# Kernel tuning notes

Hardware: AMD Instinct MI355X
Metric: run time of the kernel (lower is better)

## Reference

```python
import jax, jax.numpy as jnp
import numpy as np

HIDDEN_DIM = 2048
NUM_HEADS = 16
HEAD_DIM = HIDDEN_DIM // NUM_HEADS


def setup_inputs() -> dict:
    key = jax.random.key(0)
    ks = jax.random.split(key, 5)
    B, S, D = 1, 4096, HIDDEN_DIM
    scale = 1.0 / np.sqrt(D)
    x = jax.random.normal(ks[0], (B, S, D), dtype=jnp.float32)
    w_q = jax.random.normal(ks[1], (D, D), dtype=jnp.float32) * scale
    w_k = jax.random.normal(ks[2], (D, D), dtype=jnp.float32) * scale
    w_v = jax.random.normal(ks[3], (D, D), dtype=jnp.float32) * scale
    w_o = jax.random.normal(ks[4], (D, D), dtype=jnp.float32) * scale
    return {"x": x, "w_q": w_q, "w_k": w_k, "w_v": w_v, "w_o": w_o, "causal": 1}


def reference(x, w_q, w_k, w_v, w_o, causal):
    B, S, D = x.shape
    H, Dh = NUM_HEADS, HEAD_DIM
    sm_scale = 1.0 / np.sqrt(Dh)

    # projections (x @ W.T)
    q = jnp.einsum('bsd,ed->bse', x, w_q).reshape(B, S, H, Dh).transpose(0, 2, 1, 3)
    k = jnp.einsum('bsd,ed->bse', x, w_k).reshape(B, S, H, Dh).transpose(0, 2, 1, 3)
    v = jnp.einsum('bsd,ed->bse', x, w_v).reshape(B, S, H, Dh).transpose(0, 2, 1, 3)

    # attention scores [B, H, S, S]; flash online-softmax == standard softmax
    scores = jnp.einsum('bhqd,bhkd->bhqk', q, k) * sm_scale
    if causal:
        qpos = jnp.arange(S)[:, None]
        kpos = jnp.arange(S)[None, :]
        scores = jnp.where(qpos >= kpos, scores, -jnp.inf)
    probs = jax.nn.softmax(scores, axis=-1)
    o = jnp.einsum('bhqk,bhkd->bhqd', probs, v)  # [B, H, S, Dh]
    o = o.transpose(0, 2, 1, 3).reshape(B, S, D)
    return jnp.einsum('bsd,ed->bse', o, w_o)
```

## Files before the change

kernel.cpp:

```cpp
#include <hip/hip_runtime.h>
#include <stdint.h>

typedef __bf16 bf16_t;
typedef __bf16 bf16x8 __attribute__((ext_vector_type(8)));
typedef __bf16 bf16x4 __attribute__((ext_vector_type(4)));
typedef float  f32x4  __attribute__((ext_vector_type(4)));

static constexpr int S  = 4096;
static constexpr int D  = 2048;
static constexpr int H  = 16;
static constexpr int DH = 128;

__device__ __forceinline__ bf16x8 ld8(const bf16_t* p) { return *(const bf16x8*)p; }
__device__ __forceinline__ bf16x8 ld8c(const float* p) {
  const f32x4 a = *(const f32x4*)p;
  const f32x4 b = *(const f32x4*)(p + 4);
  bf16x8 r;
  r[0] = (bf16_t)a[0]; r[1] = (bf16_t)a[1]; r[2] = (bf16_t)a[2]; r[3] = (bf16_t)a[3];
  r[4] = (bf16_t)b[0]; r[5] = (bf16_t)b[1]; r[6] = (bf16_t)b[2]; r[7] = (bf16_t)b[3];
  return r;
}

__device__ __forceinline__ void async_ld16(const bf16_t* g, bf16_t* lds) {
  __builtin_amdgcn_global_load_lds(
      (const __attribute__((address_space(1))) uint32_t*)g,
      (__attribute__((address_space(3))) uint32_t*)lds, 16, 0, 0);
}

__global__ __launch_bounds__(256) void cvt_kernel(
    const float* __restrict__ x,  const float* __restrict__ wq,
    const float* __restrict__ wk, const float* __restrict__ wv,
    const float* __restrict__ wo,
    bf16_t* __restrict__ xb,  bf16_t* __restrict__ wqb,
    bf16_t* __restrict__ wkb, bf16_t* __restrict__ wvb,
    bf16_t* __restrict__ wob) {
  const int z = blockIdx.z;
  const float* src; bf16_t* dst; size_t off = 0;
  if      (z == 0) { src = x;  dst = xb;  off = 0; }
  else if (z == 1) { src = x;  dst = xb;  off = 4194304; }
  else if (z == 2) { src = wq; dst = wqb; }
  else if (z == 3) { src = wk; dst = wkb; }
  else if (z == 4) { src = wv; dst = wvb; }
  else             { src = wo; dst = wob; }
  const size_t i = off + ((size_t)blockIdx.x * 256 + threadIdx.x) * 8;
  *(bf16x8*)(dst + i) = ld8c(src + i);
}

template <typename TC, bool TR>
__device__ __forceinline__ void gemm_async(const bf16_t* __restrict__ A,
                                           const bf16_t* __restrict__ W,
                                           TC* __restrict__ C) {
  constexpr int K  = D;
  constexpr int BK = 32;
  __shared__ __align__(16) bf16_t Ash[128 * BK];
  __shared__ __align__(16) bf16_t Bsh[128 * BK];
  const int tid = threadIdx.x;
  const int w = tid >> 6, lane = tid & 63;
  const int c = lane & 15, g = lane >> 4;
  const int wm = w >> 1, wn = w & 1;
  const int rowBase = blockIdx.y * 128;
  const int colBase = blockIdx.x * 128;

  f32x4 acc[4][4] = {};

  for (int k0 = 0; k0 < K; k0 += BK) {
    __syncthreads();
    #pragma unroll
    for (int r = 0; r < 2; ++r) {
      const int cid = r * 256 + tid;
      const int row = cid >> 2, q = cid & 3;
      async_ld16(A + (size_t)(rowBase + row) * K + k0 + q * 8,
                 Ash + r * 2048 + w * 512);
      async_ld16(W + (size_t)(colBase + row) * K + k0 + q * 8,
                 Bsh + r * 2048 + w * 512);
    }
    __syncthreads();

    bf16x8 af[4], bf[4];
    #pragma unroll
    for (int i = 0; i < 4; ++i) af[i] = ld8(Ash + (wm * 64 + i * 16 + c) * BK + g * 8);
    #pragma unroll
    for (int j = 0; j < 4; ++j) bf[j] = ld8(Bsh + (wn * 64 + j * 16 + c) * BK + g * 8);
    #pragma unroll
    for (int i = 0; i < 4; ++i)
      #pragma unroll
      for (int j = 0; j < 4; ++j)
        acc[i][j] = __builtin_amdgcn_mfma_f32_16x16x32_bf16(af[i], bf[j], acc[i][j], 0, 0, 0);
  }

  #pragma unroll
  for (int i = 0; i < 4; ++i)
    #pragma unroll
    for (int j = 0; j < 4; ++j) {
      if (TR) {
        const int col  = colBase + wn * 64 + j * 16 + c;
        const int row0 = rowBase + wm * 64 + i * 16 + g * 4;
        bf16x4 v;
        #pragma unroll
        for (int r = 0; r < 4; ++r) v[r] = (bf16_t)acc[i][j][r];
        *(bf16x4*)((bf16_t*)C + (size_t)col * S + row0) = v;
      } else {
        #pragma unroll
        for (int r = 0; r < 4; ++r) {
          const int row = rowBase + wm * 64 + i * 16 + g * 4 + r;
          const int col = colBase + wn * 64 + j * 16 + c;
          C[(size_t)row * D + col] = (TC)acc[i][j][r];
        }
      }
    }
}

__global__ __launch_bounds__(256) void qkv_gemm_bf16(
    const bf16_t* __restrict__ X,
    const bf16_t* __restrict__ Wq, const bf16_t* __restrict__ Wk,
    const bf16_t* __restrict__ Wv,
    bf16_t* __restrict__ Qo, bf16_t* __restrict__ Ko, bf16_t* __restrict__ VTo,
    int* __restrict__ ctr) {
  if (blockIdx.x == 0 && blockIdx.y == 0 && blockIdx.z == 0 && threadIdx.x == 0)
    atomicExch(ctr, 0);
  if (blockIdx.z == 0)      gemm_async<bf16_t, false>(X, Wq, Qo);
  else if (blockIdx.z == 1) gemm_async<bf16_t, false>(X, Wk, Ko);
  else                      gemm_async<bf16_t, true >(X, Wv, VTo);
}

__global__ __launch_bounds__(256) void out_gemm_bf16(
    const bf16_t* __restrict__ A, const bf16_t* __restrict__ W,
    float* __restrict__ C) {
  gemm_async<float, false>(A, W, C);
}

__global__ __launch_bounds__(256, 2) void attn_kernel(
    const bf16_t* __restrict__ Q, const bf16_t* __restrict__ Kb,
    const bf16_t* __restrict__ VTg, bf16_t* __restrict__ O,
    const int* __restrict__ causal_p, int* __restrict__ ctr) {
  constexpr int LDK = 40;
  __shared__ __align__(16) bf16_t Ksh[4 * 64 * LDK];
  __shared__ __align__(16) bf16_t Vt[2 * 128 * LDK];
  __shared__ __align__(16) bf16_t Psh[4 * 2 * 32 * LDK];
  __shared__ int item_s;

  const int tid = threadIdx.x, w = tid >> 6, lane = tid & 63;
  const int c = lane & 15, g = lane >> 4;
  const int causal = causal_p[0];
  constexpr float QS = 0.08838834764831845f * 1.4426950408889634f;

  int knA[4], d0A[4], dV[4], kcV[4];
  #pragma unroll
  for (int r = 0; r < 4; ++r) {
    const int cid = r * 256 + tid;
    knA[r] = cid >> 4; d0A[r] = (cid & 15) * 8;
    dV[r]  = cid >> 3; kcV[r] = cid & 7;
  }

  bf16x8 onesf;
  #pragma unroll
  for (int e = 0; e < 8; ++e) onesf[e] = (c == 0) ? (bf16_t)1.0f : (bf16_t)0.0f;

  while (true) {
    __syncthreads();
    if (tid == 0) item_s = atomicAdd(ctr, 1);
    __syncthreads();
    const int it = item_s;
    if (it >= 512) break;
    const int t = causal ? (31 - (it >> 4)) : (it >> 4);
    const int h = it & 15;
    const int wrow = t * 128 + w * 32;
    const int ktiles = causal ? (2 * t + 2) : 64;

    bf16x8 qf[2][4];
    #pragma unroll
    for (int i = 0; i < 2; ++i)
      #pragma unroll
      for (int kf = 0; kf < 4; ++kf) {
        const bf16x8 raw = ld8(Q + (size_t)(wrow + i * 16 + c) * D + h * DH + kf * 32 + g * 8);
        bf16x8 sc;
        #pragma unroll
        for (int e = 0; e < 8; ++e) sc[e] = (bf16_t)((float)raw[e] * QS);
        qf[i][kf] = sc;
      }

    f32x4 o_acc[2][8] = {};
    f32x4 o_l[2] = {};

    bf16x8 kreg[4], vreg[4];
    #pragma unroll
    for (int r = 0; r < 4; ++r) {
      kreg[r] = ld8(Kb + (size_t)(0 + knA[r]) * D + h * DH + d0A[r]);
      vreg[r] = ld8(VTg + (size_t)(h * DH + dV[r]) * S + 0 + kcV[r] * 8);
    }

    for (int kt = 0; kt < ktiles; ++kt) {
      __syncthreads();
      #pragma unroll
      for (int r = 0; r < 4; ++r) {
        *(bf16x8*)(Ksh + (d0A[r] >> 5) * (64 * LDK) + knA[r] * LDK + (d0A[r] & 31)) = kreg[r];
        *(bf16x8*)(Vt + (kcV[r] >> 2) * (128 * LDK) + dV[r] * LDK + (kcV[r] & 3) * 8) = vreg[r];
      }
      __syncthreads();
      if (kt + 1 < ktiles) {
        #pragma unroll
        for (int r = 0; r < 4; ++r) {
          kreg[r] = ld8(Kb + (size_t)((kt + 1) * 64 + knA[r]) * D + h * DH + d0A[r]);
          vreg[r] = ld8(VTg + (size_t)(h * DH + dV[r]) * S + (kt + 1) * 64 + kcV[r] * 8);
        }
      }

      const bool active = !causal || (kt * 64 <= wrow + 31);
      if (active) {
        f32x4 s[2][4] = {};
        #pragma unroll
        for (int nf = 0; nf < 4; ++nf) {
          bf16x8 kk[4];
          #pragma unroll
          for (int kf = 0; kf < 4; ++kf)
            kk[kf] = ld8(Ksh + kf * (64 * LDK) + (nf * 16 + c) * LDK + g * 8);
          #pragma unroll
          for (int i = 0; i < 2; ++i)
            #pragma unroll
            for (int kf = 0; kf < 4; ++kf)
              s[i][nf] = __builtin_amdgcn_mfma_f32_16x16x32_bf16(qf[i][kf], kk[kf], s[i][nf], 0, 0, 0);
        }

        if (causal && (kt * 64 + 63 > wrow)) {
          #pragma unroll
          for (int i = 0; i < 2; ++i)
            #pragma unroll
            for (int nf = 0; nf < 4; ++nf)
              #pragma unroll
              for (int r = 0; r < 4; ++r) {
                const int kc2 = kt * 64 + nf * 16 + c;
                const int qr = wrow + i * 16 + g * 4 + r;
                if (kc2 > qr) s[i][nf][r] = -1e30f;
              }
        }

        #pragma unroll
        for (int i = 0; i < 2; ++i)
          #pragma unroll
          for (int r = 0; r < 4; ++r) {
            const int qr = i * 16 + g * 4 + r;
            #pragma unroll
            for (int nf = 0; nf < 4; ++nf) {
              const float pv = exp2f(s[i][nf][r]);
              Psh[w * (2 * 32 * LDK) + (nf >> 1) * (32 * LDK) + qr * LDK + (nf & 1) * 16 + c] = (bf16_t)pv;
            }
          }

        #pragma unroll
        for (int kf2 = 0; kf2 < 2; ++kf2) {
          bf16x8 pf[2];
          #pragma unroll
          for (int i = 0; i < 2; ++i)
            pf[i] = ld8(Psh + w * (2 * 32 * LDK) + kf2 * (32 * LDK) + (i * 16 + c) * LDK + g * 8);
          #pragma unroll
          for (int i = 0; i < 2; ++i)
            o_l[i] = __builtin_amdgcn_mfma_f32_16x16x32_bf16(pf[i], onesf, o_l[i], 0, 0, 0);
          #pragma unroll
          for (int nf = 0; nf < 8; ++nf) {
            const bf16x8 vf = ld8(Vt + kf2 * (128 * LDK) + (nf * 16 + c) * LDK + g * 8);
            #pragma unroll
            for (int i = 0; i < 2; ++i)
              o_acc[i][nf] = __builtin_amdgcn_mfma_f32_16x16x32_bf16(pf[i], vf, o_acc[i][nf], 0, 0, 0);
          }
        }
      }
    }

    #pragma unroll
    for (int i = 0; i < 2; ++i)
      #pragma unroll
      for (int r = 0; r < 4; ++r) {
        const float lv = __shfl(o_l[i][r], lane & 48, 64);
        const float inv = 1.0f / lv;
        const int row = wrow + i * 16 + g * 4 + r;
        #pragma unroll
        for (int nf = 0; nf < 8; ++nf)
          O[(size_t)row * D + h * DH + nf * 16 + c] = (bf16_t)(o_acc[i][nf][r] * inv);
      }
  }
}

extern "C" void kernel_launch(void* const* d_in, const int* in_sizes, int n_in,
                              void* d_out, int out_size, void* d_ws, size_t ws_size,
                              hipStream_t stream) {
  const float* x  = (const float*)d_in[0];
  const float* wq = (const float*)d_in[1];
  const float* wk = (const float*)d_in[2];
  const float* wv = (const float*)d_in[3];
  const float* wo = (const float*)d_in[4];
  const int* causal = (const int*)d_in[5];
  float* out = (float*)d_out;

  bf16_t* Qb  = (bf16_t*)d_ws;
  bf16_t* Kb  = Qb + (size_t)S * D;
  bf16_t* VTb = Kb + (size_t)S * D;
  bf16_t* Ob  = VTb + (size_t)S * D;
  bf16_t* xb  = Ob + (size_t)S * D;
  bf16_t* wqb = xb + (size_t)S * D;
  bf16_t* wkb = wqb + (size_t)D * D;
  bf16_t* wvb = wkb + (size_t)D * D;
  bf16_t* wob = wvb + (size_t)D * D;
  int*    ctr = (int*)(wob + (size_t)D * D);

  dim3 blk(256);
  cvt_kernel<<<dim3(2048, 1, 6), blk, 0, stream>>>(x, wq, wk, wv, wo,
                                                   xb, wqb, wkb, wvb, wob);
  qkv_gemm_bf16<<<dim3(D / 128, S / 128, 3), blk, 0, stream>>>(xb, wqb, wkb, wvb,
                                                               Qb, Kb, VTb, ctr);
  attn_kernel<<<dim3(512), blk, 0, stream>>>(Qb, Kb, VTb, Ob, causal, ctr);
  out_gemm_bf16<<<dim3(D / 128, S / 128), blk, 0, stream>>>(Ob, wob, out);
}
```

Measured before the change: 448.6 us.

## Split attention key tile across wave pairs with LDS reduction of partial outputs

The attention block grows to 512 threads (8 waves). Each pair of waves shares a 32-row query slice and takes one 32-column half of each 64-key tile, and the two partial O and row-sum accumulators are combined through LDS in two phases at the end. The causal work order also changes from longest-first to a mixed schedule. The goal is more waves in flight to hide latency and finer causal skipping per half tile. In exchange it adds extra syncs and an LDS reduction, and the new launch bounds may constrain registers.

```diff
diff --git a/kernel.cpp b/kernel.cpp
--- a/kernel.cpp
+++ b/kernel.cpp
@@ -129,25 +129,27 @@
   gemm_async<float, false>(A, W, C);
 }
 
-__global__ __launch_bounds__(256, 2) void attn_kernel(
+__global__ __launch_bounds__(512, 4) void attn_kernel(
     const bf16_t* __restrict__ Q, const bf16_t* __restrict__ Kb,
     const bf16_t* __restrict__ VTg, bf16_t* __restrict__ O,
     const int* __restrict__ causal_p, int* __restrict__ ctr) {
   constexpr int LDK = 40;
-  __shared__ __align__(16) bf16_t Ksh[4 * 64 * LDK];
-  __shared__ __align__(16) bf16_t Vt[2 * 128 * LDK];
-  __shared__ __align__(16) bf16_t Psh[4 * 2 * 32 * LDK];
+  __shared__ __align__(16) bf16_t smem[(4 * 64 + 2 * 128 + 8 * 32) * LDK];
+  bf16_t* const Ksh = smem;
+  bf16_t* const Vt  = smem + 4 * 64 * LDK;
+  bf16_t* const Psh = smem + (4 * 64 + 2 * 128) * LDK;
   __shared__ int item_s;
 
   const int tid = threadIdx.x, w = tid >> 6, lane = tid & 63;
   const int c = lane & 15, g = lane >> 4;
+  const int wq = w >> 1, wk = w & 1;
   const int causal = causal_p[0];
   constexpr float QS = 0.08838834764831845f * 1.4426950408889634f;
 
-  int knA[4], d0A[4], dV[4], kcV[4];
+  int knA[2], d0A[2], dV[2], kcV[2];
   #pragma unroll
-  for (int r = 0; r < 4; ++r) {
-    const int cid = r * 256 + tid;
+  for (int r = 0; r < 2; ++r) {
+    const int cid = r * 512 + tid;
     knA[r] = cid >> 4; d0A[r] = (cid & 15) * 8;
     dV[r]  = cid >> 3; kcV[r] = cid & 7;
   }
@@ -155,6 +157,8 @@
   bf16x8 onesf;
   #pragma unroll
   for (int e = 0; e < 8; ++e) onesf[e] = (c == 0) ? (bf16_t)1.0f : (bf16_t)0.0f;
+
+  bf16_t* const PshW = Psh + w * (32 * LDK);
 
   while (true) {
     __syncthreads();
@@ -162,9 +166,10 @@
     __syncthreads();
     const int it = item_s;
     if (it >= 512) break;
-    const int t = causal ? (31 - (it >> 4)) : (it >> 4);
+    const int jj = it >> 4;
+    const int t = causal ? ((jj < 16) ? (31 - jj) : (jj - 16)) : jj;
     const int h = it & 15;
-    const int wrow = t * 128 + w * 32;
+    const int wrow = t * 128 + wq * 32;
     const int ktiles = causal ? (2 * t + 2) : 64;
 
     bf16x8 qf[2][4];
@@ -182,53 +187,49 @@
     f32x4 o_acc[2][8] = {};
     f32x4 o_l[2] = {};
 
-    bf16x8 kreg[4], vreg[4];
-    #pragma unroll
-    for (int r = 0; r < 4; ++r) {
-      kreg[r] = ld8(Kb + (size_t)(0 + knA[r]) * D + h * DH + d0A[r]);
-      vreg[r] = ld8(VTg + (size_t)(h * DH + dV[r]) * S + 0 + kcV[r] * 8);
+    bf16x8 kreg[2], vreg[2];
+    #pragma unroll
+    for (int r = 0; r < 2; ++r) {
+      kreg[r] = ld8(Kb + (size_t)knA[r] * D + h * DH + d0A[r]);
+      vreg[r] = ld8(VTg + (size_t)(h * DH + dV[r]) * S + kcV[r] * 8);
     }
 
     for (int kt = 0; kt < ktiles; ++kt) {
       __syncthreads();
       #pragma unroll
-      for (int r = 0; r < 4; ++r) {
+      for (int r = 0; r < 2; ++r) {
         *(bf16x8*)(Ksh + (d0A[r] >> 5) * (64 * LDK) + knA[r] * LDK + (d0A[r] & 31)) = kreg[r];
         *(bf16x8*)(Vt + (kcV[r] >> 2) * (128 * LDK) + dV[r] * LDK + (kcV[r] & 3) * 8) = vreg[r];
       }
       __syncthreads();
       if (kt + 1 < ktiles) {
         #pragma unroll
-        for (int r = 0; r < 4; ++r) {
+        for (int r = 0; r < 2; ++r) {
           kreg[r] = ld8(Kb + (size_t)((kt + 1) * 64 + knA[r]) * D + h * DH + d0A[r]);
           vreg[r] = ld8(VTg + (size_t)(h * DH + dV[r]) * S + (kt + 1) * 64 + kcV[r] * 8);
         }
       }
 
-      const bool active = !causal || (kt * 64 <= wrow + 31);
+      const bool active = !causal || (kt * 64 + wk * 32 <= wrow + 31);
       if (active) {
-        f32x4 s[2][4] = {};
-        #pragma unroll
-        for (int nf = 0; nf < 4; ++nf) {
-          bf16x8 kk[4];
-          #pragma unroll
-          for (int kf = 0; kf < 4; ++kf)
-            kk[kf] = ld8(Ksh + kf * (64 * LDK) + (nf * 16 + c) * LDK + g * 8);
+        f32x4 s[2][2] = {};
+        #pragma unroll
+        for (int nf = 0; nf < 2; ++nf)
+          #pragma unroll
+          for (int kf = 0; kf < 4; ++kf) {
+            const bf16x8 kk = ld8(Ksh + kf * (64 * LDK) + (wk * 32 + nf * 16 + c) * LDK + g * 8);
+            s[0][nf] = __builtin_amdgcn_mfma_f32_16x16x32_bf16(qf[0][kf], kk, s[0][nf], 0, 0, 0);
+            s[1][nf] = __builtin_amdgcn_mfma_f32_16x16x32_bf16(qf[1][kf], kk, s[1][nf], 0, 0, 0);
+          }
+
+        if (causal && (kt * 64 + wk * 32 + 31 > wrow)) {
           #pragma unroll
           for (int i = 0; i < 2; ++i)
             #pragma unroll
-            for (int kf = 0; kf < 4; ++kf)
-              s[i][nf] = __builtin_amdgcn_mfma_f32_16x16x32_bf16(qf[i][kf], kk[kf], s[i][nf], 0, 0, 0);
-        }
-
-        if (causal && (kt * 64 + 63 > wrow)) {
-          #pragma unroll
-          for (int i = 0; i < 2; ++i)
-            #pragma unroll
-            for (int nf = 0; nf < 4; ++nf)
+            for (int nf = 0; nf < 2; ++nf)
               #pragma unroll
               for (int r = 0; r < 4; ++r) {
-                const int kc2 = kt * 64 + nf * 16 + c;
+                const int kc2 = kt * 64 + wk * 32 + nf * 16 + c;
                 const int qr = wrow + i * 16 + g * 4 + r;
                 if (kc2 > qr) s[i][nf][r] = -1e30f;
               }
@@ -240,43 +241,68 @@
           for (int r = 0; r < 4; ++r) {
             const int qr = i * 16 + g * 4 + r;
             #pragma unroll
-            for (int nf = 0; nf < 4; ++nf) {
+            for (int nf = 0; nf < 2; ++nf) {
               const float pv = exp2f(s[i][nf][r]);
-              Psh[w * (2 * 32 * LDK) + (nf >> 1) * (32 * LDK) + qr * LDK + (nf & 1) * 16 + c] = (bf16_t)pv;
+              PshW[qr * LDK + nf * 16 + c] = (bf16_t)pv;
             }
           }
 
-        #pragma unroll
-        for (int kf2 = 0; kf2 < 2; ++kf2) {
-          bf16x8 pf[2];
+        bf16x8 pf[2];
+        #pragma unroll
+        for (int i = 0; i < 2; ++i)
+          pf[i] = ld8(PshW + (i * 16 + c) * LDK + g * 8);
+        #pragma unroll
+        for (int i = 0; i < 2; ++i)
+          o_l[i] = __builtin_amdgcn_mfma_f32_16x16x32_bf16(pf[i], onesf, o_l[i], 0, 0, 0);
+        #pragma unroll
+        for (int nf = 0; nf < 8; ++nf) {
+          const bf16x8 vf = ld8(Vt + wk * (128 * LDK) + (nf * 16 + c) * LDK + g * 8);
           #pragma unroll
           for (int i = 0; i < 2; ++i)
-            pf[i] = ld8(Psh + w * (2 * 32 * LDK) + kf2 * (32 * LDK) + (i * 16 + c) * LDK + g * 8);
-          #pragma unroll
-          for (int i = 0; i < 2; ++i)
-            o_l[i] = __builtin_amdgcn_mfma_f32_16x16x32_bf16(pf[i], onesf, o_l[i], 0, 0, 0);
-          #pragma unroll
-          for (int nf = 0; nf < 8; ++nf) {
-            const bf16x8 vf = ld8(Vt + kf2 * (128 * LDK) + (nf * 16 + c) * LDK + g * 8);
-            #pragma unroll
-            for (int i = 0; i < 2; ++i)
-              o_acc[i][nf] = __builtin_amdgcn_mfma_f32_16x16x32_bf16(pf[i], vf, o_acc[i][nf], 0, 0, 0);
-          }
-        }
-      }
-    }
-
-    #pragma unroll
-    for (int i = 0; i < 2; ++i)
+            o_acc[i][nf] = __builtin_amdgcn_mfma_f32_16x16x32_bf16(pf[i], vf, o_acc[i][nf], 0, 0, 0);
+        }
+      }
+    }
+
+    float* const scratch = (float*)smem;
+    float* const myslot = scratch + (size_t)((wq & 1) * 64 + lane) * 72;
+    #pragma unroll
+    for (int phase = 0; phase < 2; ++phase) {
+      __syncthreads();
+      if ((wq >> 1) == phase && wk == 1) {
+        #pragma unroll
+        for (int i = 0; i < 2; ++i) {
+          #pragma unroll
+          for (int nf = 0; nf < 8; ++nf)
+            *(f32x4*)(myslot + (i * 8 + nf) * 4) = o_acc[i][nf];
+          *(f32x4*)(myslot + 64 + i * 4) = o_l[i];
+        }
+      }
+      __syncthreads();
+      if ((wq >> 1) == phase && wk == 0) {
+        #pragma unroll
+        for (int i = 0; i < 2; ++i) {
+          #pragma unroll
+          for (int nf = 0; nf < 8; ++nf)
+            o_acc[i][nf] += *(const f32x4*)(myslot + (i * 8 + nf) * 4);
+          o_l[i] += *(const f32x4*)(myslot + 64 + i * 4);
+        }
+      }
+    }
+
+    if (wk == 0) {
       #pragma unroll
-      for (int r = 0; r < 4; ++r) {
-        const float lv = __shfl(o_l[i][r], lane & 48, 64);
-        const float inv = 1.0f / lv;
-        const int row = wrow + i * 16 + g * 4 + r;
-        #pragma unroll
-        for (int nf = 0; nf < 8; ++nf)
-          O[(size_t)row * D + h * DH + nf * 16 + c] = (bf16_t)(o_acc[i][nf][r] * inv);
-      }
+      for (int i = 0; i < 2; ++i)
+        #pragma unroll
+        for (int r = 0; r < 4; ++r) {
+          const float lv = __shfl(o_l[i][r], lane & 48, 64);
+          const float inv = 1.0f / lv;
+          const int row = wrow + i * 16 + g * 4 + r;
+          #pragma unroll
+          for (int nf = 0; nf < 8; ++nf)
+            O[(size_t)row * D + h * DH + nf * 16 + c] = (bf16_t)(o_acc[i][nf][r] * inv);
+        }
+    }
   }
 }
 
@@ -307,6 +333,6 @@
                                                    xb, wqb, wkb, wvb, wob);
   qkv_gemm_bf16<<<dim3(D / 128, S / 128, 3), blk, 0, stream>>>(xb, wqb, wkb, wvb,
                                                                Qb, Kb, VTb, ctr);
-  attn_kernel<<<dim3(512), blk, 0, stream>>>(Qb, Kb, VTb, Ob, causal, ctr);
+  attn_kernel<<<dim3(512), dim3(512), 0, stream>>>(Qb, Kb, VTb, Ob, causal, ctr);
   out_gemm_bf16<<<dim3(D / 128, S / 128), blk, 0, stream>>>(Ob, wob, out);
 }
```

Result: slower. 961.8 us (+114.4%).

## Make attention warps independent with per-warp work items and direct global K/V loads

Applied to the files above, without the earlier changes.

Each warp now claims its own 32-row query block through a lane-0 atomic, instead of a 256-thread block claiming a 128-row tile. K and V fragments are read straight from global memory into registers, which removes the shared K/V staging and both __syncthreads per key tile. The goal is to drop block-wide barriers and let each warp stop at its own causal bound, which balances work better. In exchange, K/V reuse across the four warps of a block now relies on L1/L2 instead of LDS, and the global reads are strided and less coalesced.

```diff
diff --git a/kernel.cpp b/kernel.cpp
--- a/kernel.cpp
+++ b/kernel.cpp
@@ -134,38 +134,37 @@
     const bf16_t* __restrict__ VTg, bf16_t* __restrict__ O,
     const int* __restrict__ causal_p, int* __restrict__ ctr) {
   constexpr int LDK = 40;
-  __shared__ __align__(16) bf16_t Ksh[4 * 64 * LDK];
-  __shared__ __align__(16) bf16_t Vt[2 * 128 * LDK];
   __shared__ __align__(16) bf16_t Psh[4 * 2 * 32 * LDK];
-  __shared__ int item_s;
 
   const int tid = threadIdx.x, w = tid >> 6, lane = tid & 63;
   const int c = lane & 15, g = lane >> 4;
   const int causal = causal_p[0];
   constexpr float QS = 0.08838834764831845f * 1.4426950408889634f;
 
-  int knA[4], d0A[4], dV[4], kcV[4];
-  #pragma unroll
-  for (int r = 0; r < 4; ++r) {
-    const int cid = r * 256 + tid;
-    knA[r] = cid >> 4; d0A[r] = (cid & 15) * 8;
-    dV[r]  = cid >> 3; kcV[r] = cid & 7;
-  }
-
   bf16x8 onesf;
   #pragma unroll
   for (int e = 0; e < 8; ++e) onesf[e] = (c == 0) ? (bf16_t)1.0f : (bf16_t)0.0f;
 
+  bf16_t* const PshW = Psh + w * (2 * 32 * LDK);
+
   while (true) {
-    __syncthreads();
-    if (tid == 0) item_s = atomicAdd(ctr, 1);
-    __syncthreads();
-    const int it = item_s;
-    if (it >= 512) break;
-    const int t = causal ? (31 - (it >> 4)) : (it >> 4);
-    const int h = it & 15;
-    const int wrow = t * 128 + w * 32;
-    const int ktiles = causal ? (2 * t + 2) : 64;
+    int it;
+    if (lane == 0) it = atomicAdd(ctr, 1);
+    it = __shfl(it, 0, 64);
+    if (it >= 2048) break;
+
+    int rg, h;
+    if (causal) {
+      const int q = it >> 2, sub = it & 3;
+      const int u = q & 255, hi = q >> 8;
+      const int rq = hi ? (u & 31) : (31 - (u & 31));
+      h  = (hi << 3) | (u >> 5);
+      rg = rq * 4 + sub;
+    } else {
+      h = it >> 7; rg = it & 127;
+    }
+    const int wrow = rg * 32;
+    const int ktiles = causal ? ((wrow >> 6) + 1) : (S / 64);
 
     bf16x8 qf[2][4];
     #pragma unroll
@@ -182,86 +181,64 @@
     f32x4 o_acc[2][8] = {};
     f32x4 o_l[2] = {};
 
-    bf16x8 kreg[4], vreg[4];
-    #pragma unroll
-    for (int r = 0; r < 4; ++r) {
-      kreg[r] = ld8(Kb + (size_t)(0 + knA[r]) * D + h * DH + d0A[r]);
-      vreg[r] = ld8(VTg + (size_t)(h * DH + dV[r]) * S + 0 + kcV[r] * 8);
-    }
-
     for (int kt = 0; kt < ktiles; ++kt) {
-      __syncthreads();
-      #pragma unroll
-      for (int r = 0; r < 4; ++r) {
-        *(bf16x8*)(Ksh + (d0A[r] >> 5) * (64 * LDK) + knA[r] * LDK + (d0A[r] & 31)) = kreg[r];
-        *(bf16x8*)(Vt + (kcV[r] >> 2) * (128 * LDK) + dV[r] * LDK + (kcV[r] & 3) * 8) = vreg[r];
-      }
-      __syncthreads();
-      if (kt + 1 < ktiles) {
+      f32x4 s[2][4] = {};
+      #pragma unroll
+      for (int nf = 0; nf < 4; ++nf) {
+        bf16x8 kk[4];
+        #pragma unroll
+        for (int kf = 0; kf < 4; ++kf)
+          kk[kf] = ld8(Kb + (size_t)(kt * 64 + nf * 16 + c) * D + h * DH + kf * 32 + g * 8);
+        #pragma unroll
+        for (int kf = 0; kf < 4; ++kf) {
+          s[0][nf] = __builtin_amdgcn_mfma_f32_16x16x32_bf16(qf[0][kf], kk[kf], s[0][nf], 0, 0, 0);
+          s[1][nf] = __builtin_amdgcn_mfma_f32_16x16x32_bf16(qf[1][kf], kk[kf], s[1][nf], 0, 0, 0);
+        }
+      }
+
+      if (causal && (kt * 64 + 63 > wrow)) {
+        #pragma unroll
+        for (int i = 0; i < 2; ++i)
+          #pragma unroll
+          for (int nf = 0; nf < 4; ++nf)
+            #pragma unroll
+            for (int r = 0; r < 4; ++r) {
+              const int kc2 = kt * 64 + nf * 16 + c;
+              const int qr = wrow + i * 16 + g * 4 + r;
+              if (kc2 > qr) s[i][nf][r] = -1e30f;
+            }
+      }
+
+      #pragma unroll
+      for (int i = 0; i < 2; ++i)
         #pragma unroll
         for (int r = 0; r < 4; ++r) {
-          kreg[r] = ld8(Kb + (size_t)((kt + 1) * 64 + knA[r]) * D + h * DH + d0A[r]);
-          vreg[r] = ld8(VTg + (size_t)(h * DH + dV[r]) * S + (kt + 1) * 64 + kcV[r] * 8);
-        }
-      }
-
-      const bool active = !causal || (kt * 64 <= wrow + 31);
-      if (active) {
-        f32x4 s[2][4] = {};
-        #pragma unroll
-        for (int nf = 0; nf < 4; ++nf) {
-          bf16x8 kk[4];
+          const int qr = i * 16 + g * 4 + r;
           #pragma unroll
-          for (int kf = 0; kf < 4; ++kf)
-            kk[kf] = ld8(Ksh + kf * (64 * LDK) + (nf * 16 + c) * LDK + g * 8);
+          for (int nf = 0; nf < 4; ++nf) {
+            const float pv = exp2f(s[i][nf][r]);
+            PshW[(nf >> 1) * (32 * LDK) + qr * LDK + (nf & 1) * 16 + c] = (bf16_t)pv;
+          }
+        }
+
+      #pragma unroll
+      for (int kf2 = 0; kf2 < 2; ++kf2) {
+        bf16x8 pf[2];
+        #pragma unroll
+        for (int i = 0; i < 2; ++i)
+          pf[i] = ld8(PshW + kf2 * (32 * LDK) + (i * 16 + c) * LDK + g * 8);
+        bf16x8 vf[8];
+        #pragma unroll
+        for (int nf = 0; nf < 8; ++nf)
+          vf[nf] = ld8(VTg + (size_t)(h * DH + nf * 16 + c) * S + kt * 64 + kf2 * 32 + g * 8);
+        #pragma unroll
+        for (int i = 0; i < 2; ++i)
+          o_l[i] = __builtin_amdgcn_mfma_f32_16x16x32_bf16(pf[i], onesf, o_l[i], 0, 0, 0);
+        #pragma unroll
+        for (int nf = 0; nf < 8; ++nf) {
           #pragma unroll
           for (int i = 0; i < 2; ++i)
-            #pragma unroll
-            for (int kf = 0; kf < 4; ++kf)
-              s[i][nf] = __builtin_amdgcn_mfma_f32_16x16x32_bf16(qf[i][kf], kk[kf], s[i][nf], 0, 0, 0);
-        }
-
-        if (causal && (kt * 64 + 63 > wrow)) {
-          #pragma unroll
-          for (int i = 0; i < 2; ++i)
-            #pragma unroll
-            for (int nf = 0; nf < 4; ++nf)
-              #pragma unroll
-              for (int r = 0; r < 4; ++r) {
-                const int kc2 = kt * 64 + nf * 16 + c;
-                const int qr = wrow + i * 16 + g * 4 + r;
-                if (kc2 > qr) s[i][nf][r] = -1e30f;
-              }
-        }
-
-        #pragma unroll
-        for (int i = 0; i < 2; ++i)
-          #pragma unroll
-          for (int r = 0; r < 4; ++r) {
-            const int qr = i * 16 + g * 4 + r;
-            #pragma unroll
-            for (int nf = 0; nf < 4; ++nf) {
-              const float pv = exp2f(s[i][nf][r]);
-              Psh[w * (2 * 32 * LDK) + (nf >> 1) * (32 * LDK) + qr * LDK + (nf & 1) * 16 + c] = (bf16_t)pv;
-            }
-          }
-
-        #pragma unroll
-        for (int kf2 = 0; kf2 < 2; ++kf2) {
-          bf16x8 pf[2];
-          #pragma unroll
-          for (int i = 0; i < 2; ++i)
-            pf[i] = ld8(Psh + w * (2 * 32 * LDK) + kf2 * (32 * LDK) + (i * 16 + c) * LDK + g * 8);
-          #pragma unroll
-          for (int i = 0; i < 2; ++i)
-            o_l[i] = __builtin_amdgcn_mfma_f32_16x16x32_bf16(pf[i], onesf, o_l[i], 0, 0, 0);
-          #pragma unroll
-          for (int nf = 0; nf < 8; ++nf) {
-            const bf16x8 vf = ld8(Vt + kf2 * (128 * LDK) + (nf * 16 + c) * LDK + g * 8);
-            #pragma unroll
-            for (int i = 0; i < 2; ++i)
-              o_acc[i][nf] = __builtin_amdgcn_mfma_f32_16x16x32_bf16(pf[i], vf, o_acc[i][nf], 0, 0, 0);
-          }
+            o_acc[i][nf] = __builtin_amdgcn_mfma_f32_16x16x32_bf16(pf[i], vf[nf], o_acc[i][nf], 0, 0, 0);
         }
       }
     }
```

Measured after the change: 753.3 us. 67.9% more time.
